# Kernel optimization log

Hardware: AMD Instinct MI355X
Metric: run time of the kernel (lower is better)

Reference implementation:

```python
import jax, jax.numpy as jnp
import numpy as np
from jax import lax

T, B, F, H, C = 1024, 128, 88, 1024, 88


def setup_inputs() -> dict:
    key = jax.random.key(0)
    ks = jax.random.split(key, 8)
    s = 0.02
    lengths = jnp.sort(jax.random.randint(ks[1], (B,), 1, T + 1))[::-1]  # descending, as pack_padded requires
    return {
        "input_sequences": jax.random.normal(ks[0], (T, B, F), dtype=jnp.float32),
        "input_sequence_lengths": lengths.astype(jnp.int64),
        "W_ih": jax.random.normal(ks[2], (4 * H, F), dtype=jnp.float32) * s,
        "W_hh": jax.random.normal(ks[3], (4 * H, H), dtype=jnp.float32) * s,
        "b_ih": jax.random.normal(ks[4], (4 * H,), dtype=jnp.float32) * s,
        "b_hh": jax.random.normal(ks[5], (4 * H,), dtype=jnp.float32) * s,
        "W_fc": jax.random.normal(ks[6], (C, H), dtype=jnp.float32) * s,
        "b_fc": jax.random.normal(ks[7], (C,), dtype=jnp.float32) * s,
    }


def reference(input_sequences, input_sequence_lengths, W_ih, W_hh, b_ih, b_hh, W_fc, b_fc):
    Tn, Bn, _ = input_sequences.shape
    Hn = W_hh.shape[1]
    # mask[t, b] = True iff timestep t is within sequence b (equivalent to :batch_size_t slicing
    # when lengths are sorted descending, as the torch code assumes)
    mask_seq = jnp.arange(Tn)[:, None] < input_sequence_lengths[None, :]  # [T, B]

    h0 = jnp.zeros((Bn, Hn), dtype=input_sequences.dtype)
    c0 = jnp.zeros((Bn, Hn), dtype=input_sequences.dtype)

    def step(carry, inp):
        h, c = carry
        x, m = inp  # x: [B, F], m: [B]
        gates = x @ W_ih.T + b_ih + h @ W_hh.T + b_hh  # [B, 4H], order i,f,g,o
        i, f, g, o = jnp.split(gates, 4, axis=1)
        c_new = jax.nn.sigmoid(f) * c + jax.nn.sigmoid(i) * jnp.tanh(g)
        h_new = jax.nn.sigmoid(o) * jnp.tanh(c_new)
        mb = m[:, None]
        h2 = jnp.where(mb, h_new, h)
        c2 = jnp.where(mb, c_new, c)
        logits_t = jnp.where(mb, h2 @ W_fc.T + b_fc, 0.0)  # rows beyond batch_size_t stay zero
        return (h2, c2), logits_t

    (_, _), predictions = lax.scan(step, (h0, c0), (input_sequences, mask_seq))  # [T, B, C]

    logits = jnp.transpose(predictions, (1, 0, 2))  # [B, T, C]
    binary_logits = jnp.stack((logits, 1.0 - logits), axis=3)  # [B, T, C, 2]
    return binary_logits.reshape(-1, 2)
```

## Files before the change

kernel.cpp:

```cpp
#include <hip/hip_runtime.h>
#include <cstdint>
#include <cstddef>

#define T_STEPS 1024
#define B_SZ    128
#define F_SZ    88
#define H_SZ    1024
#define C_SZ    88

#define N_GATE_WG 128
#define N_FC_WG   3
#define N_COMPUTE (N_GATE_WG + N_FC_WG)
#define N_WG      N_COMPUTE
#define BLOCK     256
#define FLAG_STRIDE 16
#define RING      16

typedef __attribute__((ext_vector_type(8)))  __bf16 bf16x8;
typedef __attribute__((ext_vector_type(16))) float  f32x16;
typedef __attribute__((ext_vector_type(4)))  int    i32x4;

#define SLAB_OFF    0
#define SLAB_BYTES  (70 * 512 * 2)
#define BIAS_OFF    (SLAB_OFF + SLAB_BYTES)
#define LENL_OFF    (BIAS_OFF + 128)
#define NB_OFF      (LENL_OFF + 512)
#define EXCH_OFF    (NB_OFF + 2064)
#define EXCH_WAVE   (16 * 68 * 4)
#define EXCH_BYTES  (4 * EXCH_WAVE)
#define STAGE_OFF   (EXCH_OFF + EXCH_BYTES)
#define STAGE_BYTES (4 * 32 * 8 * 2)
#define SMEM_BYTES  (STAGE_OFF + STAGE_BYTES)

#define HBUF_ELEMS  131072
#define HBUF_BYTES  (HBUF_ELEMS * 2)

__device__ __forceinline__ float sigm(float x) {
    return __builtin_amdgcn_rcpf(1.0f + __expf(-x));
}
__device__ __forceinline__ float tanh_fast(float x) {
    return 1.0f - 2.0f * __builtin_amdgcn_rcpf(__expf(2.0f * x) + 1.0f);
}
__device__ __forceinline__ void st_llc(void* p, uint64_t v) {
    __hip_atomic_store((uint64_t*)p, v, __ATOMIC_RELAXED,
                       __HIP_MEMORY_SCOPE_AGENT);
}

extern "C" __global__ void __launch_bounds__(BLOCK, 1)
lstm_fused(const float* __restrict__ X,
           const int*   __restrict__ len_raw,
           const float* __restrict__ W_ih,
           const float* __restrict__ W_hh,
           const float* __restrict__ b_ih,
           const float* __restrict__ b_hh,
           const float* __restrict__ W_fc,
           const float* __restrict__ b_fc,
           float*       __restrict__ out,
           __bf16*      __restrict__ hbuf,
           int*         __restrict__ flags)
{
    extern __shared__ char smem[];
    __bf16*         slab  = (__bf16*)(smem + SLAB_OFF);
    float*          biasL = (float*)(smem + BIAS_OFF);
    int*            lenL  = (int*)(smem + LENL_OFF);
    unsigned short* nbL   = (unsigned short*)(smem + NB_OFF);

    const int  wg   = blockIdx.x;
    const int  tid  = threadIdx.x;
    const int  w    = tid >> 6;
    const int  lane = tid & 63;
    const int  col  = lane & 31;
    const int  h5   = lane >> 5;
    const bool isGate = (wg < N_GATE_WG);

    const int lstride = (len_raw[1] == 0) ? 2 : 1;
    if (tid < B_SZ) lenL[tid] = len_raw[tid * lstride];
    __syncthreads();
    for (int t = tid; t <= T_STEPS; t += BLOCK) {
        int cnt = 0;
        #pragma unroll 4
        for (int b = 0; b < B_SZ; ++b) cnt += (lenL[b] > t) ? 1 : 0;
        nbL[t] = (unsigned short)cnt;
    }

    if (isGate) {
        const int j0 = wg * 8;
        for (int idx = tid; idx < 32 * 1024; idx += BLOCK) {
            int cc = idx >> 10, k = idx & 1023;
            int gate = cc & 3, u = cc >> 2;
            float v = W_hh[(size_t)(gate * H_SZ + j0 + u) * H_SZ + k];
            slab[((k >> 4) * 64 + ((k >> 3) & 1) * 32 + cc) * 8 + (k & 7)] = (__bf16)v;
        }
        for (int idx = tid; idx < 32 * 96; idx += BLOCK) {
            int cc = idx & 31, k = idx >> 5;
            int gate = cc & 3, u = cc >> 2;
            float v = (k < F_SZ) ? W_ih[(size_t)(gate * H_SZ + j0 + u) * F_SZ + k] : 0.0f;
            slab[((64 + (k >> 4)) * 64 + ((k >> 3) & 1) * 32 + cc) * 8 + (k & 7)] = (__bf16)v;
        }
        if (tid < 32) {
            int gate = tid & 3, u = tid >> 2;
            int row = gate * H_SZ + j0 + u;
            biasL[tid] = b_ih[row] + b_hh[row];
        }
    } else {
        const int c0 = (wg - N_GATE_WG) * 32;
        for (int idx = tid; idx < 32 * 1024; idx += BLOCK) {
            int cc = idx >> 10, k = idx & 1023;
            int c = c0 + cc;
            float v = (c < C_SZ) ? W_fc[(size_t)c * H_SZ + k] : 0.0f;
            slab[((k >> 4) * 64 + ((k >> 3) & 1) * 32 + cc) * 8 + (k & 7)] = (__bf16)v;
        }
        if (tid < 32) {
            int c = c0 + tid;
            biasL[tid] = (c < C_SZ) ? b_fc[c] : 0.0f;
        }
    }

    __syncthreads();
    if (tid == 0) {
        __builtin_amdgcn_s_waitcnt(0);
        __hip_atomic_store(flags + wg * FLAG_STRIDE, 1, __ATOMIC_RELAXED,
                           __HIP_MEMORY_SCOPE_AGENT);
    }

    float c_reg[4] = {0.f, 0.f, 0.f, 0.f};
    float h_reg[4] = {0.f, 0.f, 0.f, 0.f};

    const int g4    = col & 3;
    const int ktile = wg >> 1;
    const int half  = wg & 1;
    const int u0    = col >> 2;
    const int c0fc  = (wg - N_GATE_WG) * 32;
    const int phase = wg & (RING - 1);

    float*  exch   = (float*)(smem + EXCH_OFF) + w * (EXCH_WAVE / 4);
    __bf16* stageW = (__bf16*)(smem + STAGE_OFF) + w * 256;

    const bool has2 = (128 + lane) < N_COMPUTE;
    long guard = 0;

    for (int t = 0; t <= T_STEPS; ++t) {
        const int nb_t   = (t < T_STEPS) ? (int)nbL[t] : 0;
        const int nb_pre = (t > 0) ? (int)nbL[t - 1] : B_SZ;
        const __bf16* hin  = hbuf + (size_t)((t + RING - 1) & (RING - 1)) * HBUF_ELEMS;
        __bf16*       hout = hbuf + (size_t)(t & (RING - 1)) * HBUF_ELEMS;

        const bool gcomp = isGate && (t < T_STEPS) && (w * 32 < nb_t);
        const bool gwrt  = isGate && (t < T_STEPS) && (w * 32 < nb_pre);

        f32x16 acc;

        if (gcomp) {
            float bv = biasL[col];
            #pragma unroll
            for (int i = 0; i < 16; ++i) acc[i] = bv;
            const float* xrow = X + ((size_t)t * B_SZ + (w * 32 + col)) * F_SZ;
            #pragma unroll
            for (int kt = 0; kt < 6; ++kt) {
                int f0 = kt * 16 + h5 * 8;
                bf16x8 a;
                if (f0 < F_SZ) {
                    float4 lo = *(const float4*)(xrow + f0);
                    float4 hi = *(const float4*)(xrow + f0 + 4);
                    a[0] = (__bf16)lo.x; a[1] = (__bf16)lo.y; a[2] = (__bf16)lo.z; a[3] = (__bf16)lo.w;
                    a[4] = (__bf16)hi.x; a[5] = (__bf16)hi.y; a[6] = (__bf16)hi.z; a[7] = (__bf16)hi.w;
                } else {
                    #pragma unroll
                    for (int j = 0; j < 8; ++j) a[j] = (__bf16)0.0f;
                }
                bf16x8 b = __builtin_bit_cast(bf16x8,
                    *(const i32x4*)(slab + (size_t)(64 + kt) * 512 + lane * 8));
                acc = __builtin_amdgcn_mfma_f32_32x32x16_bf16(a, b, acc, 0, 0, 0);
            }
        }

        if (w == 0) {
            const int target = t + 1;
            for (;;) {
                int a = __hip_atomic_load(flags + lane * FLAG_STRIDE,
                                          __ATOMIC_RELAXED, __HIP_MEMORY_SCOPE_AGENT);
                int b = __hip_atomic_load(flags + (64 + lane) * FLAG_STRIDE,
                                          __ATOMIC_RELAXED, __HIP_MEMORY_SCOPE_AGENT);
                int c = has2 ? __hip_atomic_load(flags + (128 + lane) * FLAG_STRIDE,
                                                 __ATOMIC_RELAXED, __HIP_MEMORY_SCOPE_AGENT)
                             : target;
                if (__all((a >= target) && (b >= target) && (c >= target))) break;
                __builtin_amdgcn_s_sleep(1);
                if (++guard > 400000000L) break;
            }
        }
        __syncthreads();

        if (((t + phase) & (RING - 1)) == 0) {
            if (tid == 0)
                __builtin_amdgcn_fence(__ATOMIC_ACQUIRE, "agent");
            __syncthreads();
        }

        if (!isGate && tid == 0) {
            __hip_atomic_store(flags + wg * FLAG_STRIDE, t + 2, __ATOMIC_RELAXED,
                               __HIP_MEMORY_SCOPE_AGENT);
        }

        if (!isGate && t >= 1) {
            const int  s        = t - 1;
            const int  nb_s     = (int)nbL[s];
            const bool act_tile = (w * 32) < nb_s;
            #pragma unroll
            for (int i = 0; i < 16; ++i) acc[i] = 0.0f;
            if (act_tile) {
                float bv = biasL[col];
                #pragma unroll
                for (int i = 0; i < 16; ++i) acc[i] = bv;
                const __bf16* hA = hbuf + (size_t)((t + RING - 1) & (RING - 1)) * HBUF_ELEMS
                                        + (size_t)(w * 64 + lane) * 8;
                const __bf16* bB = slab + lane * 8;
                #pragma unroll 8
                for (int kt = 0; kt < 64; ++kt) {
                    bf16x8 a = __builtin_bit_cast(bf16x8, *(const i32x4*)(hA + (size_t)kt * 2048));
                    bf16x8 b = __builtin_bit_cast(bf16x8, *(const i32x4*)(bB + (size_t)kt * 512));
                    acc = __builtin_amdgcn_mfma_f32_32x32x16_bf16(a, b, acc, 0, 0, 0);
                }
            }
            const int c = c0fc + col;
            if (c < C_SZ) {
                #pragma unroll
                for (int i = 0; i < 16; ++i) {
                    int row = (i & 3) + 8 * (i >> 2) + 4 * h5;
                    int b   = w * 32 + row;
                    float v = (act_tile && b < nb_s) ? acc[i] : 0.0f;
                    float2 o2; o2.x = v; o2.y = 1.0f - v;
                    *(float2*)(out + ((size_t)(b * T_STEPS + s) * C_SZ + c) * 2) = o2;
                }
            }
        }

        if (gcomp && t > 0) {
            const __bf16* hA = hin + (size_t)(w * 64 + lane) * 8;
            const __bf16* bB = slab + lane * 8;
            i32x4 pf0[16], pf1[16];
            #pragma unroll
            for (int i = 0; i < 16; ++i)
                pf0[i] = *(const i32x4*)(hA + (size_t)i * 2048);
            __builtin_amdgcn_sched_barrier(0);
            #pragma unroll
            for (int c = 0; c < 4; ++c) {
                i32x4 (&cur)[16] = (c & 1) ? pf1 : pf0;
                i32x4 (&nxt)[16] = (c & 1) ? pf0 : pf1;
                if (c < 3) {
                    #pragma unroll
                    for (int i = 0; i < 16; ++i)
                        nxt[i] = *(const i32x4*)(hA + (size_t)((c + 1) * 16 + i) * 2048);
                }
                __builtin_amdgcn_sched_barrier(0);
                #pragma unroll
                for (int i = 0; i < 16; ++i) {
                    bf16x8 a = __builtin_bit_cast(bf16x8, cur[i]);
                    bf16x8 b = __builtin_bit_cast(bf16x8,
                        *(const i32x4*)(bB + (size_t)(c * 16 + i) * 512));
                    acc = __builtin_amdgcn_mfma_f32_32x32x16_bf16(a, b, acc, 0, 0, 0);
                }
                __builtin_amdgcn_sched_barrier(0);
            }
        }
        if (gcomp) {
            #pragma unroll
            for (int j = 0; j < 16; ++j) exch[j * 68 + lane] = acc[j];
        }
        __syncthreads();

        if (gcomp) {
            #pragma unroll
            for (int q = 0; q < 4; ++q) {
                const float4 v = *(const float4*)(exch + (4 * g4 + q) * 68 + 32 * h5 + (col & ~3));
                float si = sigm(v.x);
                float sf = sigm(v.y);
                float tg = tanh_fast(v.z);
                float so = sigm(v.w);
                float cn = sf * c_reg[q] + si * tg;
                float hn = so * tanh_fast(cn);
                int row = 8 * g4 + 4 * h5 + q;
                int b   = w * 32 + row;
                if (b < nb_t) { c_reg[q] = cn; h_reg[q] = hn; }
            }
        }
        if (gwrt) {
            #pragma unroll
            for (int q = 0; q < 4; ++q) {
                int row = 8 * g4 + 4 * h5 + q;
                stageW[row * 8 + u0] = (__bf16)h_reg[q];
            }
        }
        __syncthreads();

        if (gwrt && h5 == half) {
            const uint64_t* sp = (const uint64_t*)(stageW + col * 8);
            uint64_t* hp = (uint64_t*)(hout + (size_t)((ktile * 4 + w) * 64 + half * 32 + col) * 8);
            st_llc(hp,     sp[0]);
            st_llc(hp + 1, sp[1]);
        }
        __syncthreads();

        if (isGate && tid == 0) {
            __builtin_amdgcn_s_waitcnt(0);
            __hip_atomic_store(flags + wg * FLAG_STRIDE, t + 2, __ATOMIC_RELAXED,
                               __HIP_MEMORY_SCOPE_AGENT);
        }
    }
}

extern "C" void kernel_launch(void* const* d_in, const int* in_sizes, int n_in,
                              void* d_out, int out_size, void* d_ws, size_t ws_size,
                              hipStream_t stream) {
    const float* X    = (const float*)d_in[0];
    const int*   lens = (const int*)d_in[1];
    const float* Wih  = (const float*)d_in[2];
    const float* Whh  = (const float*)d_in[3];
    const float* bih  = (const float*)d_in[4];
    const float* bhh  = (const float*)d_in[5];
    const float* Wfc  = (const float*)d_in[6];
    const float* bfc  = (const float*)d_in[7];
    float*       outp = (float*)d_out;

    __bf16* hbuf  = (__bf16*)d_ws;
    int*    flags = (int*)((char*)d_ws + (size_t)RING * HBUF_BYTES);

    (void)hipFuncSetAttribute((const void*)lstm_fused,
                              hipFuncAttributeMaxDynamicSharedMemorySize, SMEM_BYTES);

    void* args[] = { (void*)&X, (void*)&lens, (void*)&Wih, (void*)&Whh,
                     (void*)&bih, (void*)&bhh, (void*)&Wfc, (void*)&bfc,
                     (void*)&outp, (void*)&hbuf, (void*)&flags };
    hipError_t le = hipLaunchCooperativeKernel((void*)lstm_fused, dim3(N_WG), dim3(BLOCK),
                                               args, (unsigned)SMEM_BYTES, stream);
    if (le != hipSuccess) {
        hipLaunchKernelGGL(lstm_fused, dim3(N_WG), dim3(BLOCK),
                           (unsigned)SMEM_BYTES, stream,
                           X, lens, Wih, Whh, bih, bhh, Wfc, bfc, outp, hbuf, flags);
    }
}
```

Before: 8.570 ms.

## Repartition LSTM gate work: 16 units per WG, two batch halves, split barriers

```diff
diff --git a/kernel.cpp b/kernel.cpp
--- a/kernel.cpp
+++ b/kernel.cpp
@@ -9,10 +9,10 @@
 #define C_SZ    88
 
 #define N_GATE_WG 128
-#define N_FC_WG   3
+#define N_FC_WG   6
 #define N_COMPUTE (N_GATE_WG + N_FC_WG)
 #define N_WG      N_COMPUTE
-#define BLOCK     256
+#define BLOCK     128
 #define FLAG_STRIDE 16
 #define RING      16
 
@@ -21,16 +21,14 @@
 typedef __attribute__((ext_vector_type(4)))  int    i32x4;
 
 #define SLAB_OFF    0
-#define SLAB_BYTES  (70 * 512 * 2)
+#define SLAB_BYTES  (64 * 1024 * 2)
 #define BIAS_OFF    (SLAB_OFF + SLAB_BYTES)
-#define LENL_OFF    (BIAS_OFF + 128)
+#define LENL_OFF    (BIAS_OFF + 256)
 #define NB_OFF      (LENL_OFF + 512)
 #define EXCH_OFF    (NB_OFF + 2064)
-#define EXCH_WAVE   (16 * 68 * 4)
-#define EXCH_BYTES  (4 * EXCH_WAVE)
-#define STAGE_OFF   (EXCH_OFF + EXCH_BYTES)
-#define STAGE_BYTES (4 * 32 * 8 * 2)
-#define SMEM_BYTES  (STAGE_OFF + STAGE_BYTES)
+#define EXCH_WAVE   (32 * 68 * 4)
+#define STAGE_OFF   (EXCH_OFF + 2 * EXCH_WAVE)
+#define SMEM_BYTES  (STAGE_OFF + 2 * 512 * 2)
 
 #define HBUF_ELEMS  131072
 #define HBUF_BYTES  (HBUF_ELEMS * 2)
@@ -73,6 +71,13 @@
     const int  h5   = lane >> 5;
     const bool isGate = (wg < N_GATE_WG);
 
+    int ug = 0, bt2 = 0, cg = 0;
+    if (isGate) { int m = wg >> 3, x = wg & 7; bt2 = x >> 2; ug = 4 * m + (x & 3); }
+    else        { int f = wg - N_GATE_WG; bt2 = f / 3; cg = f % 3; }
+    const int bti  = bt2 * 2 + w;
+    const int fidx = bt2 * 68 + (isGate ? ug : (64 + cg));
+    const int hbase = bt2 * 68;
+
     const int lstride = (len_raw[1] == 0) ? 2 : 1;
     if (tid < B_SZ) lenL[tid] = len_raw[tid * lstride];
     __syncthreads();
@@ -83,35 +88,48 @@
         nbL[t] = (unsigned short)cnt;
     }
 
+    bf16x8 wih[2][6];
     if (isGate) {
-        const int j0 = wg * 8;
+        for (int idx = tid; idx < 64 * 1024; idx += BLOCK) {
+            int cc2 = idx >> 10, k = idx & 1023;
+            int n = cc2 >> 5, cc = cc2 & 31;
+            int gate = cc & 3, ul = cc >> 2;
+            int j = ug * 16 + n * 8 + ul;
+            float v = W_hh[(size_t)(gate * H_SZ + j) * H_SZ + k];
+            slab[(size_t)((k >> 4) * 128 + n * 64 + ((k >> 3) & 1) * 32 + cc) * 8 + (k & 7)] = (__bf16)v;
+        }
+        {
+            const int gate = col & 3, ul = col >> 2;
+            #pragma unroll
+            for (int n = 0; n < 2; ++n) {
+                const float* wrow = W_ih + (size_t)(gate * H_SZ + ug * 16 + n * 8 + ul) * F_SZ;
+                #pragma unroll
+                for (int kt = 0; kt < 6; ++kt) {
+                    const int f0 = kt * 16 + h5 * 8;
+                    bf16x8 b;
+                    #pragma unroll
+                    for (int e = 0; e < 8; ++e) {
+                        int k = f0 + e;
+                        b[e] = (k < F_SZ) ? (__bf16)wrow[k] : (__bf16)0.0f;
+                    }
+                    wih[n][kt] = b;
+                }
+            }
+        }
+        if (tid < 64) {
+            int n = tid >> 5, cc = tid & 31, gate = cc & 3, ul = cc >> 2;
+            int row = gate * H_SZ + ug * 16 + n * 8 + ul;
+            biasL[tid] = b_ih[row] + b_hh[row];
+        }
+    } else {
         for (int idx = tid; idx < 32 * 1024; idx += BLOCK) {
             int cc = idx >> 10, k = idx & 1023;
-            int gate = cc & 3, u = cc >> 2;
-            float v = W_hh[(size_t)(gate * H_SZ + j0 + u) * H_SZ + k];
-            slab[((k >> 4) * 64 + ((k >> 3) & 1) * 32 + cc) * 8 + (k & 7)] = (__bf16)v;
-        }
-        for (int idx = tid; idx < 32 * 96; idx += BLOCK) {
-            int cc = idx & 31, k = idx >> 5;
-            int gate = cc & 3, u = cc >> 2;
-            float v = (k < F_SZ) ? W_ih[(size_t)(gate * H_SZ + j0 + u) * F_SZ + k] : 0.0f;
-            slab[((64 + (k >> 4)) * 64 + ((k >> 3) & 1) * 32 + cc) * 8 + (k & 7)] = (__bf16)v;
+            int c = cg * 32 + cc;
+            float v = (c < C_SZ) ? W_fc[(size_t)c * H_SZ + k] : 0.0f;
+            slab[(size_t)((k >> 4) * 64 + ((k >> 3) & 1) * 32 + cc) * 8 + (k & 7)] = (__bf16)v;
         }
         if (tid < 32) {
-            int gate = tid & 3, u = tid >> 2;
-            int row = gate * H_SZ + j0 + u;
-            biasL[tid] = b_ih[row] + b_hh[row];
-        }
-    } else {
-        const int c0 = (wg - N_GATE_WG) * 32;
-        for (int idx = tid; idx < 32 * 1024; idx += BLOCK) {
-            int cc = idx >> 10, k = idx & 1023;
-            int c = c0 + cc;
-            float v = (c < C_SZ) ? W_fc[(size_t)c * H_SZ + k] : 0.0f;
-            slab[((k >> 4) * 64 + ((k >> 3) & 1) * 32 + cc) * 8 + (k & 7)] = (__bf16)v;
-        }
-        if (tid < 32) {
-            int c = c0 + tid;
+            int c = cg * 32 + tid;
             biasL[tid] = (c < C_SZ) ? b_fc[c] : 0.0f;
         }
     }
@@ -119,25 +137,23 @@
     __syncthreads();
     if (tid == 0) {
         __builtin_amdgcn_s_waitcnt(0);
-        __hip_atomic_store(flags + wg * FLAG_STRIDE, 1, __ATOMIC_RELAXED,
+        __hip_atomic_store(flags + fidx * FLAG_STRIDE, 1, __ATOMIC_RELAXED,
                            __HIP_MEMORY_SCOPE_AGENT);
     }
 
-    float c_reg[4] = {0.f, 0.f, 0.f, 0.f};
-    float h_reg[4] = {0.f, 0.f, 0.f, 0.f};
-
-    const int g4    = col & 3;
-    const int ktile = wg >> 1;
-    const int half  = wg & 1;
+    const int a4    = col & 3;
     const int u0    = col >> 2;
-    const int c0fc  = (wg - N_GATE_WG) * 32;
+    const int c0fc  = cg * 32;
     const int phase = wg & (RING - 1);
 
     float*  exch   = (float*)(smem + EXCH_OFF) + w * (EXCH_WAVE / 4);
-    __bf16* stageW = (__bf16*)(smem + STAGE_OFF) + w * 256;
-
-    const bool has2 = (128 + lane) < N_COMPUTE;
+    __bf16* stageW = (__bf16*)(smem + STAGE_OFF) + w * 512;
+
+    const bool hasFC = (lane < 3);
     long guard = 0;
+
+    float c_reg[8] = {0.f,0.f,0.f,0.f,0.f,0.f,0.f,0.f};
+    float h_reg[8] = {0.f,0.f,0.f,0.f,0.f,0.f,0.f,0.f};
 
     for (int t = 0; t <= T_STEPS; ++t) {
         const int nb_t   = (t < T_STEPS) ? (int)nbL[t] : 0;
@@ -145,16 +161,19 @@
         const __bf16* hin  = hbuf + (size_t)((t + RING - 1) & (RING - 1)) * HBUF_ELEMS;
         __bf16*       hout = hbuf + (size_t)(t & (RING - 1)) * HBUF_ELEMS;
 
-        const bool gcomp = isGate && (t < T_STEPS) && (w * 32 < nb_t);
-        const bool gwrt  = isGate && (t < T_STEPS) && (w * 32 < nb_pre);
-
-        f32x16 acc;
+        const bool gcomp = isGate && (t < T_STEPS) && (bti * 32 < nb_t);
+        const bool gwrt  = isGate && (t < T_STEPS) && (bti * 32 < nb_pre);
+
+        f32x16 acc[2];
 
         if (gcomp) {
-            float bv = biasL[col];
-            #pragma unroll
-            for (int i = 0; i < 16; ++i) acc[i] = bv;
-            const float* xrow = X + ((size_t)t * B_SZ + (w * 32 + col)) * F_SZ;
+            #pragma unroll
+            for (int n = 0; n < 2; ++n) {
+                float bv = biasL[n * 32 + col];
+                #pragma unroll
+                for (int i = 0; i < 16; ++i) acc[n][i] = bv;
+            }
+            const float* xrow = X + ((size_t)t * B_SZ + (bti * 32 + col)) * F_SZ;
             #pragma unroll
             for (int kt = 0; kt < 6; ++kt) {
                 int f0 = kt * 16 + h5 * 8;
@@ -168,23 +187,21 @@
                     #pragma unroll
                     for (int j = 0; j < 8; ++j) a[j] = (__bf16)0.0f;
                 }
-                bf16x8 b = __builtin_bit_cast(bf16x8,
-                    *(const i32x4*)(slab + (size_t)(64 + kt) * 512 + lane * 8));
-                acc = __builtin_amdgcn_mfma_f32_32x32x16_bf16(a, b, acc, 0, 0, 0);
+                #pragma unroll
+                for (int n = 0; n < 2; ++n)
+                    acc[n] = __builtin_amdgcn_mfma_f32_32x32x16_bf16(a, wih[n][kt], acc[n], 0, 0, 0);
             }
         }
 
         if (w == 0) {
             const int target = t + 1;
             for (;;) {
-                int a = __hip_atomic_load(flags + lane * FLAG_STRIDE,
+                int a = __hip_atomic_load(flags + (hbase + lane) * FLAG_STRIDE,
                                           __ATOMIC_RELAXED, __HIP_MEMORY_SCOPE_AGENT);
-                int b = __hip_atomic_load(flags + (64 + lane) * FLAG_STRIDE,
-                                          __ATOMIC_RELAXED, __HIP_MEMORY_SCOPE_AGENT);
-                int c = has2 ? __hip_atomic_load(flags + (128 + lane) * FLAG_STRIDE,
-                                                 __ATOMIC_RELAXED, __HIP_MEMORY_SCOPE_AGENT)
-                             : target;
-                if (__all((a >= target) && (b >= target) && (c >= target))) break;
+                int b = hasFC ? __hip_atomic_load(flags + (hbase + 64 + lane) * FLAG_STRIDE,
+                                                  __ATOMIC_RELAXED, __HIP_MEMORY_SCOPE_AGENT)
+                              : target;
+                if (__all((a >= target) && (b >= target))) break;
                 __builtin_amdgcn_s_sleep(1);
                 if (++guard > 400000000L) break;
             }
@@ -198,28 +215,28 @@
         }
 
         if (!isGate && tid == 0) {
-            __hip_atomic_store(flags + wg * FLAG_STRIDE, t + 2, __ATOMIC_RELAXED,
+            __hip_atomic_store(flags + fidx * FLAG_STRIDE, t + 2, __ATOMIC_RELAXED,
                                __HIP_MEMORY_SCOPE_AGENT);
         }
 
         if (!isGate && t >= 1) {
             const int  s        = t - 1;
             const int  nb_s     = (int)nbL[s];
-            const bool act_tile = (w * 32) < nb_s;
-            #pragma unroll
-            for (int i = 0; i < 16; ++i) acc[i] = 0.0f;
+            const bool act_tile = (bti * 32) < nb_s;
+            f32x16 accf;
+            #pragma unroll
+            for (int i = 0; i < 16; ++i) accf[i] = 0.0f;
             if (act_tile) {
                 float bv = biasL[col];
                 #pragma unroll
-                for (int i = 0; i < 16; ++i) acc[i] = bv;
-                const __bf16* hA = hbuf + (size_t)((t + RING - 1) & (RING - 1)) * HBUF_ELEMS
-                                        + (size_t)(w * 64 + lane) * 8;
+                for (int i = 0; i < 16; ++i) accf[i] = bv;
+                const __bf16* hA = hin + (size_t)bti * 512 + (size_t)lane * 8;
                 const __bf16* bB = slab + lane * 8;
                 #pragma unroll 8
                 for (int kt = 0; kt < 64; ++kt) {
                     bf16x8 a = __builtin_bit_cast(bf16x8, *(const i32x4*)(hA + (size_t)kt * 2048));
                     bf16x8 b = __builtin_bit_cast(bf16x8, *(const i32x4*)(bB + (size_t)kt * 512));
-                    acc = __builtin_amdgcn_mfma_f32_32x32x16_bf16(a, b, acc, 0, 0, 0);
+                    accf = __builtin_amdgcn_mfma_f32_32x32x16_bf16(a, b, accf, 0, 0, 0);
                 }
             }
             const int c = c0fc + col;
@@ -227,8 +244,8 @@
                 #pragma unroll
                 for (int i = 0; i < 16; ++i) {
                     int row = (i & 3) + 8 * (i >> 2) + 4 * h5;
-                    int b   = w * 32 + row;
-                    float v = (act_tile && b < nb_s) ? acc[i] : 0.0f;
+                    int b   = bti * 32 + row;
+                    float v = (act_tile && b < nb_s) ? accf[i] : 0.0f;
                     float2 o2; o2.x = v; o2.y = 1.0f - v;
                     *(float2*)(out + ((size_t)(b * T_STEPS + s) * C_SZ + c) * 2) = o2;
                 }
@@ -236,7 +253,7 @@
         }
 
         if (gcomp && t > 0) {
-            const __bf16* hA = hin + (size_t)(w * 64 + lane) * 8;
+            const __bf16* hA = hin + (size_t)bti * 512 + (size_t)lane * 8;
             const __bf16* bB = slab + lane * 8;
             i32x4 pf0[16], pf1[16];
             #pragma unroll
@@ -256,46 +273,55 @@
                 #pragma unroll
                 for (int i = 0; i < 16; ++i) {
                     bf16x8 a = __builtin_bit_cast(bf16x8, cur[i]);
-                    bf16x8 b = __builtin_bit_cast(bf16x8,
-                        *(const i32x4*)(bB + (size_t)(c * 16 + i) * 512));
-                    acc = __builtin_amdgcn_mfma_f32_32x32x16_bf16(a, b, acc, 0, 0, 0);
+                    const int ks = c * 16 + i;
+                    bf16x8 b0 = __builtin_bit_cast(bf16x8,
+                        *(const i32x4*)(bB + (size_t)ks * 1024));
+                    acc[0] = __builtin_amdgcn_mfma_f32_32x32x16_bf16(a, b0, acc[0], 0, 0, 0);
+                    bf16x8 b1 = __builtin_bit_cast(bf16x8,
+                        *(const i32x4*)(bB + (size_t)ks * 1024 + 512));
+                    acc[1] = __builtin_amdgcn_mfma_f32_32x32x16_bf16(a, b1, acc[1], 0, 0, 0);
                 }
                 __builtin_amdgcn_sched_barrier(0);
             }
         }
         if (gcomp) {
             #pragma unroll
-            for (int j = 0; j < 16; ++j) exch[j * 68 + lane] = acc[j];
+            for (int n = 0; n < 2; ++n)
+                #pragma unroll
+                for (int j = 0; j < 16; ++j)
+                    exch[(n * 16 + j) * 68 + lane] = acc[n][j];
         }
         __syncthreads();
 
         if (gcomp) {
             #pragma unroll
-            for (int q = 0; q < 4; ++q) {
-                const float4 v = *(const float4*)(exch + (4 * g4 + q) * 68 + 32 * h5 + (col & ~3));
-                float si = sigm(v.x);
-                float sf = sigm(v.y);
-                float tg = tanh_fast(v.z);
-                float so = sigm(v.w);
-                float cn = sf * c_reg[q] + si * tg;
-                float hn = so * tanh_fast(cn);
-                int row = 8 * g4 + 4 * h5 + q;
-                int b   = w * 32 + row;
-                if (b < nb_t) { c_reg[q] = cn; h_reg[q] = hn; }
+            for (int n = 0; n < 2; ++n) {
+                #pragma unroll
+                for (int q = 0; q < 4; ++q) {
+                    const float4 v = *(const float4*)(exch + (n * 16 + 4 * a4 + q) * 68 + 32 * h5 + (col & ~3));
+                    float si = sigm(v.x);
+                    float sf = sigm(v.y);
+                    float tg = tanh_fast(v.z);
+                    float so = sigm(v.w);
+                    float cn = sf * c_reg[n * 4 + q] + si * tg;
+                    float hn = so * tanh_fast(cn);
+                    int b = bti * 32 + 8 * a4 + 4 * h5 + q;
+                    if (b < nb_t) { c_reg[n * 4 + q] = cn; h_reg[n * 4 + q] = hn; }
+                }
             }
         }
         if (gwrt) {
             #pragma unroll
-            for (int q = 0; q < 4; ++q) {
-                int row = 8 * g4 + 4 * h5 + q;
-                stageW[row * 8 + u0] = (__bf16)h_reg[q];
-            }
+            for (int n = 0; n < 2; ++n)
+                #pragma unroll
+                for (int q = 0; q < 4; ++q)
+                    stageW[(8 * a4 + 4 * h5 + q) * 16 + n * 8 + u0] = (__bf16)h_reg[n * 4 + q];
         }
         __syncthreads();
 
-        if (gwrt && h5 == half) {
-            const uint64_t* sp = (const uint64_t*)(stageW + col * 8);
-            uint64_t* hp = (uint64_t*)(hout + (size_t)((ktile * 4 + w) * 64 + half * 32 + col) * 8);
+        if (gwrt) {
+            const uint64_t* sp = (const uint64_t*)(stageW + (size_t)col * 16 + (size_t)h5 * 8);
+            uint64_t* hp = (uint64_t*)(hout + (size_t)ug * 2048 + (size_t)bti * 512 + (size_t)lane * 8);
             st_llc(hp,     sp[0]);
             st_llc(hp + 1, sp[1]);
         }
@@ -303,7 +329,7 @@
 
         if (isGate && tid == 0) {
             __builtin_amdgcn_s_waitcnt(0);
-            __hip_atomic_store(flags + wg * FLAG_STRIDE, t + 2, __ATOMIC_RELAXED,
+            __hip_atomic_store(flags + fidx * FLAG_STRIDE, t + 2, __ATOMIC_RELAXED,
                                __HIP_MEMORY_SCOPE_AGENT);
         }
     }
```

Result: faster. 7.885 ms (-8.0%).
